# Optimization experiments

Measured on AMD Instinct MI355X. Metric: run time of the kernel, lower is better.

## Reference

```python
import jax, jax.numpy as jnp
import numpy as np

SEQ_LEN = 12          # seq_length
K = 8                 # nsamples = 2 * num_samples
RADII = (4.0 + 1e-06, 8.0 + 1e-06, 12.0 + 1e-06)
COUT = (64, 128, 256)


def _group(xyz, s_xyz, radius):
    # ball query via knn + radius mask: xyz (B,N,3) queries, s_xyz (B,M,3) keys
    d2 = jnp.sum((xyz[:, :, None, :] - s_xyz[:, None, :, :]) ** 2, axis=-1)  # (B,N,M)
    neg, idx = jax.lax.top_k(-d2, K)                                          # (B,N,K)
    valid = (-neg) <= radius * radius
    # points outside the ball are replaced by the nearest neighbor (pad-with-first)
    return jnp.where(valid, idx, idx[..., :1])


def _gather(a, idx):
    # a (B,M,C), idx (B,N,K) -> (B,N,K,C)
    return jax.vmap(lambda t, i: t[i])(a, idx)


def _cell(xyz, feat, state, W, b, radius, cout):
    # PointRNN cell: group state points around current points, fuse
    # [displacement, current feature, state feature] with a shared linear,
    # then max-pool over the K neighbors. New state xyz = current xyz.
    B, N, _ = xyz.shape
    if state is None:
        s_xyz, s_feat = xyz, jnp.zeros((B, N, cout), xyz.dtype)
    else:
        s_xyz, s_feat = state
    idx = _group(xyz, s_xyz, radius)
    n_xyz = _gather(s_xyz, idx)                      # (B,N,K,3)
    n_feat = _gather(s_feat, idx)                    # (B,N,K,cout)
    disp = n_xyz - xyz[:, :, None, :]
    parts = [disp]
    if feat is not None:
        cin = feat.shape[-1]
        parts.append(jnp.broadcast_to(feat[:, :, None, :], (B, N, K, cin)))
    parts.append(n_feat)
    h = jnp.concatenate(parts, axis=-1) @ W + b      # (B,N,K,cout)
    return (xyz, jnp.max(h, axis=2))                 # (xyz, (B,N,cout))


def _forward(frames, W1, b1, W2, b2, W3, b3, Wm, bm, Wl, bl):
    half = SEQ_LEN // 2
    s1 = s2 = s3 = None
    # encode
    for i in range(half):
        s1 = _cell(frames[:, i], None, s1, W1, b1, RADII[0], COUT[0])
        s2 = _cell(s1[0], s1[1], s2, W2, b2, RADII[1], COUT[1])
        s3 = _cell(s2[0], s2[1], s3, W3, b3, RADII[2], COUT[2])
    # decode
    input_frame = frames[:, half - 1]
    preds = []
    for i in range(half, SEQ_LEN):
        s1 = _cell(input_frame, None, s1, W1, b1, RADII[0], COUT[0])
        s2 = _cell(s1[0], s1[1], s2, W2, b2, RADII[1], COUT[1])
        s3 = _cell(s2[0], s2[1], s3, W3, b3, RADII[2], COUT[2])
        h = jax.nn.relu(s3[1] @ Wm + bm)             # MLP([256,64]) = Lin+ReLU
        motion = h @ Wl + bl                         # (B,N,3)
        input_frame = input_frame + motion
        preds.append(input_frame)
    return jnp.stack(preds, axis=1)                  # (B, T/2, N, 3)


def setup_inputs() -> dict:
    key = jax.random.key(0)
    ks = jax.random.split(key, 12)
    B, N = 16, 512
    frames = jax.random.normal(ks[0], (B, SEQ_LEN, N, 3), jnp.float32) * 2.0

    def lin(k, fin, fout):
        k1, k2 = jax.random.split(k)
        s = 1.0 / np.sqrt(fin)
        return (jax.random.uniform(k1, (fin, fout), jnp.float32, -s, s),
                jax.random.uniform(k2, (fout,), jnp.float32, -s, s))

    W1, b1 = lin(ks[1], 3 + 0 + 64, 64)
    W2, b2 = lin(ks[2], 3 + 64 + 128, 128)
    W3, b3 = lin(ks[3], 3 + 128 + 256, 256)
    Wm, bm = lin(ks[4], 256, 64)
    Wl, bl = lin(ks[5], 64, 3)
    return {"frames": frames, "W1": W1, "b1": b1, "W2": W2, "b2": b2,
            "W3": W3, "b3": b3, "Wm": Wm, "bm": bm, "Wl": Wl, "bl": bl}


def reference(frames, W1, b1, W2, b2, W3, b3, Wm, bm, Wl, bl):
    return _forward(frames, W1, b1, W2, b2, W3, b3, Wm, bm, Wl, bl)
```

## Files before the change

kernel.cpp:

```cpp
#include <hip/hip_runtime.h>
#include <hip/hip_cooperative_groups.h>
#include <math.h>

namespace cg = cooperative_groups;

#define BB 16
#define NN 512
#define KNN 8
#define SEQ 12
#define TQK 16
#define QB 32
#define PB 16

typedef __attribute__((ext_vector_type(8))) short bf8_t;
typedef __attribute__((ext_vector_type(4))) float f4_t;

__device__ __forceinline__ ushort f2b(float x) {
    uint u = __float_as_uint(x);
    return (ushort)((u + 0x7fffu + ((u >> 16) & 1u)) >> 16);
}
__device__ __forceinline__ float b2f(ushort h) {
    return __uint_as_float((uint)h << 16);
}

struct CellsSM {
    float s2s[PB][132];
    float s3f[PB][260];
    float dsp[3][PB][KNN][3];
    int   jss[3][PB][KNN];
    union { ushort s1b[2][PB][72]; float hs[PB][64]; } u1;
    ushort s2b[2][PB][136];
    ushort s3c[2][PB][264];
};
union __align__(16) SM {
    CellsSM c;
    ushort  g[384 * 40];
    float   kf[1544 + 4608 + 4608];
};
union __align__(16) GKSM {
    ushort  g[384 * 40];
    float   kf[1544 + 4608 + 4608];
};

#define GRPN 64
__device__ __forceinline__ void group_barrier(int* __restrict__ bar, int g,
                                              int target, int tid) {
    __syncthreads();
    if (tid == 0) {
        __threadfence();
        atomicAdd(&bar[g * 32], 1);
        while (__hip_atomic_load(&bar[g * 32], __ATOMIC_ACQUIRE,
                                 __HIP_MEMORY_SCOPE_AGENT) < target)
            __builtin_amdgcn_s_sleep(2);
        __threadfence();
    }
    __syncthreads();
}

__device__ __forceinline__ void knn512(
        const float* __restrict__ xqp, int xq_bs,
        const float* __restrict__ xsp, int xs_bs,
        int* __restrict__ idx1, int* __restrict__ idx2, int* __restrict__ idx3,
        float r2a, float r2b, float r2c,
        int ntile, int b, float* __restrict__ smf) {
    float* s   = smf;
    float* cdp = smf + 1544;
    int*   cip = (int*)(smf + 1544 + 4608);
    const int tid = threadIdx.x;

    {
        int j = tid;
        const float* p = xsp + (long)b * xs_bs + j * 3;
        int o = 3 * j + (j >> 6);
        s[o + 0] = p[0]; s[o + 1] = p[1]; s[o + 2] = p[2];
    }
    __syncthreads();

    int qi  = tid >> 4;
    int sub = tid & 15;
    int n = ntile * QB + qi;
    const float* q = xqp + (long)b * xq_bs + n * 3;
    float qx = q[0], qy = q[1], qz2 = q[2];

    float bd[KNN];
    int   bi[KNN];
#pragma unroll
    for (int k = 0; k < KNN; ++k) { bd[k] = 1e30f; bi[k] = 0; }

    int j0 = sub * (NN / TQK);
    int sbase = 3 * j0 + (j0 >> 6);
#pragma unroll 4
    for (int jj = 0; jj < NN / TQK; ++jj) {
        float dx = s[sbase + 3 * jj + 0] - qx;
        float dy = s[sbase + 3 * jj + 1] - qy;
        float dz = s[sbase + 3 * jj + 2] - qz2;
        float d2 = fmaf(dx, dx, fmaf(dy, dy, dz * dz));
        if (d2 < bd[KNN - 1]) {
            bd[KNN - 1] = d2; bi[KNN - 1] = j0 + jj;
#pragma unroll
            for (int k = KNN - 1; k >= 1; --k) {
                if (bd[k] < bd[k - 1]) {
                    float td = bd[k]; bd[k] = bd[k - 1]; bd[k - 1] = td;
                    int   ti = bi[k]; bi[k] = bi[k - 1]; bi[k - 1] = ti;
                }
            }
        }
    }

    float* cdq = cdp + (qi * TQK + sub) * (KNN + 1);
    int*   ciq = cip + (qi * TQK + sub) * (KNN + 1);
#pragma unroll
    for (int k = 0; k < KNN; ++k) { cdq[k] = bd[k]; ciq[k] = bi[k]; }
    cdq[KNN] = 1e30f; ciq[KNN] = 0x7fffffff;
    __syncthreads();

    for (int stride = TQK / 2; stride >= 1; stride >>= 1) {
        if (sub < stride) {
            float* ca = cdp + (qi * TQK + sub) * (KNN + 1);
            float* cb = cdp + (qi * TQK + sub + stride) * (KNN + 1);
            int*   ja_p = cip + (qi * TQK + sub) * (KNN + 1);
            int*   jb_p = cip + (qi * TQK + sub + stride) * (KNN + 1);
            float rd[KNN]; int ri[KNN];
            int ia = 0, ib = 0;
#pragma unroll
            for (int k = 0; k < KNN; ++k) {
                float da = ca[ia], db = cb[ib];
                int   ja = ja_p[ia], jb = jb_p[ib];
                bool ta = (da < db) || (da == db && ja < jb);
                rd[k] = ta ? da : db; ri[k] = ta ? ja : jb;
                ia += ta ? 1 : 0; ib += ta ? 0 : 1;
            }
#pragma unroll
            for (int k = 0; k < KNN; ++k) { ca[k] = rd[k]; ja_p[k] = ri[k]; }
        }
        __syncthreads();
    }

    if (sub == 0) {
        long base = ((long)(b * NN + n)) * KNN;
        float* c0  = cdp + qi * TQK * (KNN + 1);
        int*   j0p = cip + qi * TQK * (KNN + 1);
        int i0 = j0p[0];
#pragma unroll
        for (int k = 0; k < KNN; ++k) {
            float d = c0[k]; int j = j0p[k];
            idx1[base + k] = (d <= r2a) ? j : i0;
            idx2[base + k] = (d <= r2b) ? j : i0;
            idx3[base + k] = (d <= r2c) ? j : i0;
        }
    }
}

template<int N>
__device__ __forceinline__ void gemmTile512(
        const ushort* __restrict__ Ah, const ushort* __restrict__ Al,
        const ushort* __restrict__ Bh, const ushort* __restrict__ Bl,
        float* __restrict__ G, int rb, int cb, int tid, ushort* lds) {
    const int row0 = rb * 128, c0 = cb * 64;
    ushort* ah = lds;
    ushort* al = lds + 128 * 40;
    ushort* bh = lds + 256 * 40;
    ushort* bl = lds + 320 * 40;
    const int wv = tid >> 6, lane = tid & 63;
    const int m = lane & 15, quad = lane >> 4;
    const int lr = tid >> 2, ls = (tid & 3) * 8;
    const int lrB = lr & 63;
    ushort* bstage = (tid < 256) ? bh : bl;
    const ushort* Bsrc = (tid < 256) ? Bh : Bl;

    f4_t acc[4];
#pragma unroll
    for (int ct = 0; ct < 4; ++ct) acc[ct] = (f4_t){0.f, 0.f, 0.f, 0.f};

    bf8_t pa_h = *(const bf8_t*)(Ah + (long)(row0 + lr) * N + ls);
    bf8_t pa_l = *(const bf8_t*)(Al + (long)(row0 + lr) * N + ls);
    bf8_t pb   = *(const bf8_t*)(Bsrc + (long)(c0 + lrB) * N + ls);

    for (int k0 = 0; k0 < N; k0 += 32) {
        __syncthreads();
        *(bf8_t*)(ah + lr * 40 + ls) = pa_h;
        *(bf8_t*)(al + lr * 40 + ls) = pa_l;
        *(bf8_t*)(bstage + lrB * 40 + ls) = pb;
        __syncthreads();
        if (k0 + 32 < N) {
            int kn = k0 + 32;
            pa_h = *(const bf8_t*)(Ah + (long)(row0 + lr) * N + kn + ls);
            pa_l = *(const bf8_t*)(Al + (long)(row0 + lr) * N + kn + ls);
            pb   = *(const bf8_t*)(Bsrc + (long)(c0 + lrB) * N + kn + ls);
        }
        bf8_t a_h = *(const bf8_t*)(ah + (wv * 16 + m) * 40 + quad * 8);
        bf8_t a_l = *(const bf8_t*)(al + (wv * 16 + m) * 40 + quad * 8);
#pragma unroll
        for (int ct = 0; ct < 4; ++ct) {
            bf8_t bth = *(const bf8_t*)(bh + (ct * 16 + m) * 40 + quad * 8);
            bf8_t btl = *(const bf8_t*)(bl + (ct * 16 + m) * 40 + quad * 8);
            acc[ct] = __builtin_amdgcn_mfma_f32_16x16x32_bf16(a_h, bth, acc[ct], 0, 0, 0);
            acc[ct] = __builtin_amdgcn_mfma_f32_16x16x32_bf16(a_h, btl, acc[ct], 0, 0, 0);
            acc[ct] = __builtin_amdgcn_mfma_f32_16x16x32_bf16(a_l, bth, acc[ct], 0, 0, 0);
        }
    }
#pragma unroll
    for (int ct = 0; ct < 4; ++ct) {
        int col = c0 + ct * 16 + m;
#pragma unroll
        for (int r = 0; r < 4; ++r)
            G[(long)(row0 + wv * 16 + quad * 4 + r) * N + col] = acc[ct][r];
    }
}

__device__ __forceinline__ void cells_phase(
        bool first,
        const float* __restrict__ xq, int xq_bs,
        const float* __restrict__ xs, int xs_bs,
        const int* __restrict__ i1, const int* __restrict__ i2,
        const int* __restrict__ i3,
        const float* __restrict__ G1p, const float* __restrict__ G2p,
        const float* __restrict__ G3p,
        ushort* __restrict__ s1h, ushort* __restrict__ s1l,
        ushort* __restrict__ s2h, ushort* __restrict__ s2l,
        ushort* __restrict__ s3h, ushort* __restrict__ s3l,
        const float* __restrict__ W1, const float* __restrict__ b1,
        const float* __restrict__ W2, const float* __restrict__ b2,
        const float* __restrict__ W3, const float* __restrict__ b3,
        const ushort* __restrict__ w2fh, const ushort* __restrict__ w2fl,
        const ushort* __restrict__ w3fh, const ushort* __restrict__ w3fl,
        const ushort* __restrict__ wmh, const ushort* __restrict__ wml,
        const float* __restrict__ bm,
        const float* __restrict__ Wl, const float* __restrict__ bl,
        float* __restrict__ xnext, int xn_bs, int do_head,
        int blk, int tid, CellsSM& sm) {
    const int xcd = blk & 7, slot = blk >> 3;
    const int b   = xcd * 2 + (slot >> 5);
    const int n0  = (slot & 31) << 4;
    const long row0 = (long)b * NN + n0;
    const long bN = (long)b * NN;
    const int wv = tid >> 6, lane = tid & 63;
    const int fm = lane & 15, quad = lane >> 4;

    for (int t = tid; t < 3 * PB * KNN; t += 512) {
        int r = t >> 7, rem = t & 127, p = rem >> 3, k = rem & 7;
        const int* ix = (r == 0) ? i1 : ((r == 1) ? i2 : i3);
        int j = ix[(row0 + p) * KNN + k];
        sm.jss[r][p][k] = j;
        const float* sp = xs + (long)b * xs_bs + j * 3;
        const float* qp = xq + (long)b * xq_bs + (n0 + p) * 3;
        sm.dsp[r][p][k][0] = sp[0] - qp[0];
        sm.dsp[r][p][k][1] = sp[1] - qp[1];
        sm.dsp[r][p][k][2] = sp[2] - qp[2];
    }
    __syncthreads();

    {
        int co = tid & 63, q = tid >> 6;
        float g1r[2][KNN];
        if (!first) {
#pragma unroll
            for (int r = 0; r < 2; ++r)
#pragma unroll
                for (int k = 0; k < KNN; ++k)
                    g1r[r][k] = G1p[(bN + sm.jss[0][2 * q + r][k]) * 64 + co];
        }
        float wx = W1[co], wy = W1[64 + co], wz = W1[128 + co];
        float bz = b1[co];
#pragma unroll
        for (int r = 0; r < 2; ++r) {
            int p = 2 * q + r;
            float acc = -1e30f;
#pragma unroll
            for (int k = 0; k < KNN; ++k) {
                float v = fmaf(sm.dsp[0][p][k][0], wx, bz);
                v = fmaf(sm.dsp[0][p][k][1], wy, v);
                v = fmaf(sm.dsp[0][p][k][2], wz, v);
                if (!first) v += g1r[r][k];
                acc = fmaxf(acc, v);
            }
            ushort h = f2b(acc);
            ushort l = f2b(acc - b2f(h));
            sm.u1.s1b[0][p][co] = h;
            sm.u1.s1b[1][p][co] = l;
            s1h[(row0 + p) * 64 + co] = h;
            s1l[(row0 + p) * 64 + co] = l;
        }
    }
    __syncthreads();

    float4 g2r[KNN];
    {
        int c4 = tid & 31, g = tid >> 5;
        if (!first) {
#pragma unroll
            for (int k = 0; k < KNN; ++k)
                g2r[k] = ((const float4*)G2p)[(bN + sm.jss[1][g][k]) * 32 + c4];
        }
    }

    {
        int col = wv * 16 + fm;
        float bz = b2[col];
        f4_t acc = {bz, bz, bz, bz};
#pragma unroll
        for (int k0 = 0; k0 < 64; k0 += 32) {
            bf8_t ah = *(const bf8_t*)&sm.u1.s1b[0][fm][k0 + quad * 8];
            bf8_t al = *(const bf8_t*)&sm.u1.s1b[1][fm][k0 + quad * 8];
            bf8_t bh = *(const bf8_t*)(w2fh + col * 64 + k0 + quad * 8);
            bf8_t bl = *(const bf8_t*)(w2fl + col * 64 + k0 + quad * 8);
            acc = __builtin_amdgcn_mfma_f32_16x16x32_bf16(ah, bh, acc, 0, 0, 0);
            acc = __builtin_amdgcn_mfma_f32_16x16x32_bf16(ah, bl, acc, 0, 0, 0);
            acc = __builtin_amdgcn_mfma_f32_16x16x32_bf16(al, bh, acc, 0, 0, 0);
        }
#pragma unroll
        for (int r = 0; r < 4; ++r) sm.s2s[quad * 4 + r][col] = acc[r];
    }
    __syncthreads();

    {
        int c4 = tid & 31, g = tid >> 5;
        float4 bse = *(float4*)&sm.s2s[g][c4 * 4];
        float4 wx = ((const float4*)W2)[c4];
        float4 wy = ((const float4*)(W2 + 128))[c4];
        float4 wz = ((const float4*)(W2 + 256))[c4];
        float4 m = make_float4(-1e30f, -1e30f, -1e30f, -1e30f);
#pragma unroll
        for (int k = 0; k < KNN; ++k) {
            float dx = sm.dsp[1][g][k][0], dy = sm.dsp[1][g][k][1],
                  dz = sm.dsp[1][g][k][2];
            float4 v;
            v.x = fmaf(dz, wz.x, fmaf(dy, wy.x, fmaf(dx, wx.x, bse.x)));
            v.y = fmaf(dz, wz.y, fmaf(dy, wy.y, fmaf(dx, wx.y, bse.y)));
            v.z = fmaf(dz, wz.z, fmaf(dy, wy.z, fmaf(dx, wx.z, bse.z)));
            v.w = fmaf(dz, wz.w, fmaf(dy, wy.w, fmaf(dx, wx.w, bse.w)));
            if (!first) {
                v.x += g2r[k].x; v.y += g2r[k].y;
                v.z += g2r[k].z; v.w += g2r[k].w;
            }
            m.x = fmaxf(m.x, v.x); m.y = fmaxf(m.y, v.y);
            m.z = fmaxf(m.z, v.z); m.w = fmaxf(m.w, v.w);
        }
        ushort4 mh, ml;
        mh.x = f2b(m.x); ml.x = f2b(m.x - b2f(mh.x));
        mh.y = f2b(m.y); ml.y = f2b(m.y - b2f(mh.y));
        mh.z = f2b(m.z); ml.z = f2b(m.z - b2f(mh.z));
        mh.w = f2b(m.w); ml.w = f2b(m.w - b2f(mh.w));
        *(ushort4*)&sm.s2b[0][g][c4 * 4] = mh;
        *(ushort4*)&sm.s2b[1][g][c4 * 4] = ml;
        *(ushort4*)&s2h[(row0 + g) * 128 + c4 * 4] = mh;
        *(ushort4*)&s2l[(row0 + g) * 128 + c4 * 4] = ml;
    }
    __syncthreads();

    float4 g3r[2][KNN];
    {
        int c4 = tid & 63, g = tid >> 6;
        if (!first) {
#pragma unroll
            for (int r = 0; r < 2; ++r)
#pragma unroll
                for (int k = 0; k < KNN; ++k)
                    g3r[r][k] = ((const float4*)G3p)[(bN + sm.jss[2][2 * g + r][k]) * 64 + c4];
        }
    }

    {
        int col0 = wv * 16 + fm, col1 = (wv + 8) * 16 + fm;
        float bz0 = b3[col0], bz1 = b3[col1];
        f4_t a0 = {bz0, bz0, bz0, bz0};
        f4_t a1 = {bz1, bz1, bz1, bz1};
#pragma unroll
        for (int k0 = 0; k0 < 128; k0 += 32) {
            bf8_t ah = *(const bf8_t*)&sm.s2b[0][fm][k0 + quad * 8];
            bf8_t al = *(const bf8_t*)&sm.s2b[1][fm][k0 + quad * 8];
            bf8_t b0h = *(const bf8_t*)(w3fh + col0 * 128 + k0 + quad * 8);
            bf8_t b0l = *(const bf8_t*)(w3fl + col0 * 128 + k0 + quad * 8);
            bf8_t b1h = *(const bf8_t*)(w3fh + col1 * 128 + k0 + quad * 8);
            bf8_t b1l = *(const bf8_t*)(w3fl + col1 * 128 + k0 + quad * 8);
            a0 = __builtin_amdgcn_mfma_f32_16x16x32_bf16(ah, b0h, a0, 0, 0, 0);
            a0 = __builtin_amdgcn_mfma_f32_16x16x32_bf16(ah, b0l, a0, 0, 0, 0);
            a0 = __builtin_amdgcn_mfma_f32_16x16x32_bf16(al, b0h, a0, 0, 0, 0);
            a1 = __builtin_amdgcn_mfma_f32_16x16x32_bf16(ah, b1h, a1, 0, 0, 0);
            a1 = __builtin_amdgcn_mfma_f32_16x16x32_bf16(ah, b1l, a1, 0, 0, 0);
            a1 = __builtin_amdgcn_mfma_f32_16x16x32_bf16(al, b1h, a1, 0, 0, 0);
        }
#pragma unroll
        for (int r = 0; r < 4; ++r) {
            sm.s3f[quad * 4 + r][col0] = a0[r];
            sm.s3f[quad * 4 + r][col1] = a1[r];
        }
    }
    __syncthreads();

    {
        int c4 = tid & 63, g = tid >> 6;
        float4 wx = ((const float4*)W3)[c4];
        float4 wy = ((const float4*)(W3 + 256))[c4];
        float4 wz = ((const float4*)(W3 + 512))[c4];
#pragma unroll
        for (int r = 0; r < 2; ++r) {
            int p = 2 * g + r;
            float4 bse = *(float4*)&sm.s3f[p][c4 * 4];
            float4 m = make_float4(-1e30f, -1e30f, -1e30f, -1e30f);
#pragma unroll
            for (int k = 0; k < KNN; ++k) {
                float dx = sm.dsp[2][p][k][0], dy = sm.dsp[2][p][k][1],
                      dz = sm.dsp[2][p][k][2];
                float4 v;
                v.x = fmaf(dz, wz.x, fmaf(dy, wy.x, fmaf(dx, wx.x, bse.x)));
                v.y = fmaf(dz, wz.y, fmaf(dy, wy.y, fmaf(dx, wx.y, bse.y)));
                v.z = fmaf(dz, wz.z, fmaf(dy, wy.z, fmaf(dx, wx.z, bse.z)));
                v.w = fmaf(dz, wz.w, fmaf(dy, wy.w, fmaf(dx, wx.w, bse.w)));
                if (!first) {
                    v.x += g3r[r][k].x; v.y += g3r[r][k].y;
                    v.z += g3r[r][k].z; v.w += g3r[r][k].w;
                }
                m.x = fmaxf(m.x, v.x); m.y = fmaxf(m.y, v.y);
                m.z = fmaxf(m.z, v.z); m.w = fmaxf(m.w, v.w);
            }
            ushort4 mh, ml;
            mh.x = f2b(m.x); ml.x = f2b(m.x - b2f(mh.x));
            mh.y = f2b(m.y); ml.y = f2b(m.y - b2f(mh.y));
            mh.z = f2b(m.z); ml.z = f2b(m.z - b2f(mh.z));
            mh.w = f2b(m.w); ml.w = f2b(m.w - b2f(mh.w));
            *(ushort4*)&sm.s3c[0][p][c4 * 4] = mh;
            *(ushort4*)&sm.s3c[1][p][c4 * 4] = ml;
            *(ushort4*)&s3h[(row0 + p) * 256 + c4 * 4] = mh;
            *(ushort4*)&s3l[(row0 + p) * 256 + c4 * 4] = ml;
        }
    }

    if (do_head) {
        __syncthreads();
        if (wv < 4) {
            int col = wv * 16 + fm;
            float bz = bm[col];
            f4_t acc = {bz, bz, bz, bz};
#pragma unroll
            for (int k0 = 0; k0 < 256; k0 += 32) {
                bf8_t ah = *(const bf8_t*)&sm.s3c[0][fm][k0 + quad * 8];
                bf8_t al = *(const bf8_t*)&sm.s3c[1][fm][k0 + quad * 8];
                bf8_t bh = *(const bf8_t*)(wmh + col * 256 + k0 + quad * 8);
                bf8_t bl = *(const bf8_t*)(wml + col * 256 + k0 + quad * 8);
                acc = __builtin_amdgcn_mfma_f32_16x16x32_bf16(ah, bh, acc, 0, 0, 0);
                acc = __builtin_amdgcn_mfma_f32_16x16x32_bf16(ah, bl, acc, 0, 0, 0);
                acc = __builtin_amdgcn_mfma_f32_16x16x32_bf16(al, bh, acc, 0, 0, 0);
            }
            __syncthreads();
#pragma unroll
            for (int r = 0; r < 4; ++r)
                sm.u1.hs[quad * 4 + r][col] = fmaxf(acc[r], 0.f);
        } else {
            __syncthreads();
        }
        __syncthreads();
        if (tid < PB * 3) {
            int p = tid / 3, d = tid % 3;
            float m = bl[d];
#pragma unroll 4
            for (int c = 0; c < 64; ++c)
                m = fmaf(sm.u1.hs[p][c], Wl[c * 3 + d], m);
            const float* qp = xq + (long)b * xq_bs + (n0 + p) * 3;
            xnext[(long)b * xn_bs + (n0 + p) * 3 + d] = qp[d] + m;
        }
    }
}

__device__ __forceinline__ void convW_one(int id,
        const float* __restrict__ W1, const float* __restrict__ W2,
        const float* __restrict__ W3, const float* __restrict__ Wm,
        ushort* w1h, ushort* w1l, ushort* w2h, ushort* w2l,
        ushort* w3h, ushort* w3l, ushort* w2fh, ushort* w2fl,
        ushort* w3fh, ushort* w3fl, ushort* wmh, ushort* wml) {
    float v; ushort* ph; ushort* pl; int idx;
    if (id < 4096)        { int n = id >> 6, k = id & 63;
        v = W1[(3 + k) * 64 + n];   ph = w1h;  pl = w1l;  idx = id; }
    else if (id < 20480)  { int u = id - 4096, n = u >> 7, k = u & 127;
        v = W2[(67 + k) * 128 + n]; ph = w2h;  pl = w2l;  idx = u; }
    else if (id < 86016)  { int u = id - 20480, n = u >> 8, k = u & 255;
        v = W3[(131 + k) * 256 + n]; ph = w3h; pl = w3l;  idx = u; }
    else if (id < 94208)  { int u = id - 86016, n = u >> 6, k = u & 63;
        v = W2[(3 + k) * 128 + n];  ph = w2fh; pl = w2fl; idx = u; }
    else if (id < 126976) { int u = id - 94208, n = u >> 7, k = u & 127;
        v = W3[(3 + k) * 256 + n];  ph = w3fh; pl = w3fl; idx = u; }
    else if (id < 143360) { int u = id - 126976, n = u >> 8, k = u & 255;
        v = Wm[k * 64 + n];         ph = wmh;  pl = wml;  idx = u; }
    else return;
    ushort h = f2b(v);
    ph[idx] = h; pl[idx] = f2b(v - b2f(h));
}

__global__ __launch_bounds__(512, 4) void fused_kernel(
        const float* frames, float* out,
        float* G1, float* G2, float* G3,
        ushort* s1h, ushort* s1l, ushort* s2h, ushort* s2l,
        ushort* s3h, ushort* s3l,
        ushort* w1h, ushort* w1l, ushort* w2h, ushort* w2l,
        ushort* w3h, ushort* w3l,
        ushort* w2fh, ushort* w2fl, ushort* w3fh, ushort* w3fl,
        ushort* wmh, ushort* wml,
        int* idx1w, int* idx2w, int* idx3w, int* bar,
        const float* W1, const float* b1, const float* W2, const float* b2,
        const float* W3, const float* b3, const float* Wm, const float* bm,
        const float* Wl, const float* bl,
        float r2a, float r2b, float r2c) {
    __shared__ SM sm;
    cg::grid_group grid = cg::this_grid();
    const int bx = blockIdx.x, tid = threadIdx.x;
    const int grp = bx & 7;
    const int FB = SEQ * NN * 3, OB = 6 * NN * 3;
    const long BNK = (long)BB * NN * KNN;

    if (bx == 0 && tid < 8) bar[tid * 32] = 0;
    convW_one(bx * 512 + tid, W1, W2, W3, Wm,
              w1h, w1l, w2h, w2l, w3h, w3l,
              w2fh, w2fl, w3fh, w3fl, wmh, wml);
    if (bx < 256) {
        int xcd = bx & 7, slot = bx >> 3;
        int b = xcd * 2 + (slot & 1), ntile = slot >> 1;
        knn512(frames, FB, frames, FB, idx1w, idx2w, idx3w,
               r2a, r2b, r2c, ntile, b, sm.kf);
    }
    __threadfence();
    grid.sync();

    int ph = 1;

    for (int t = 0; t < SEQ; ++t) {
        const float* xq; int xq_bs; const float* xs; int xs_bs;
        if (t < 6)       { xq = frames + (long)t * NN * 3;        xq_bs = FB; }
        else if (t == 6) { xq = frames + 5L * NN * 3;             xq_bs = FB; }
        else             { xq = out + (long)(t - 7) * NN * 3;     xq_bs = OB; }
        if (t == 0)      { xs = xq;                               xs_bs = xq_bs; }
        else if (t <= 6) { xs = frames + (long)(t - 1) * NN * 3;  xs_bs = FB; }
        else if (t == 7) { xs = frames + 5L * NN * 3;             xs_bs = FB; }
        else             { xs = out + (long)(t - 8) * NN * 3;     xs_bs = OB; }
        int slot = (t <= 6) ? t : 0;
        const int* i1 = idx1w + slot * BNK;
        const int* i2 = idx2w + slot * BNK;
        const int* i3 = idx3w + slot * BNK;
        int do_head = (t >= 6);
        float* xnext = do_head ? out + (long)(t - 6) * NN * 3 : nullptr;

        cells_phase(t == 0, xq, xq_bs, xs, xs_bs, i1, i2, i3,
                    G1, G2, G3, s1h, s1l, s2h, s2l, s3h, s3l,
                    W1, b1, W2, b2, W3, b3,
                    w2fh, w2fl, w3fh, w3fl, wmh, wml, bm,
                    Wl, bl, xnext, OB, do_head, bx, tid, sm.c);

        if (t == SEQ - 1) break;
        group_barrier(bar, grp, GRPN * ph, tid); ++ph;

        if (bx < 256) {
            int tn = t + 1;
            const float* kq; int kq_bs; const float* ksp; int ks_bs; int kslot;
            if (tn <= 6) {
                int qz = tn < 5 ? tn : 5;
                kq = frames + (long)qz * NN * 3;        kq_bs = FB;
                ksp = frames + (long)(tn - 1) * NN * 3; ks_bs = FB;
                kslot = tn;
            } else {
                kq = out + (long)(tn - 7) * NN * 3;     kq_bs = OB;
                if (tn == 7) { ksp = frames + 5L * NN * 3;          ks_bs = FB; }
                else         { ksp = out + (long)(tn - 8) * NN * 3; ks_bs = OB; }
                kslot = 0;
            }
            int xcd = bx & 7, slot2 = bx >> 3;
            int b = xcd * 2 + (slot2 & 1), ntile = slot2 >> 1;
            knn512(kq, kq_bs, ksp, ks_bs,
                   idx1w + (long)kslot * BNK, idx2w + (long)kslot * BNK,
                   idx3w + (long)kslot * BNK,
                   r2a, r2b, r2c, ntile, b, sm.kf);
        } else {
            for (int it = bx - 256; it < 448; it += 256) {
                if (it < 256) {
                    int xcd = it & 7, rem = it >> 3;
                    int rb = xcd * 8 + (rem & 7), cb = rem >> 3;
                    gemmTile512<256>(s3h, s3l, w3h, w3l, G3, rb, cb, tid, sm.g);
                } else if (it < 384) {
                    int u = it - 256; int xcd = u & 7, rem = u >> 3;
                    int rb = xcd * 8 + (rem & 7), cb = rem >> 3;
                    gemmTile512<128>(s2h, s2l, w2h, w2l, G2, rb, cb, tid, sm.g);
                } else {
                    int u = it - 384; int xcd = u & 7, j = u >> 3;
                    gemmTile512<64>(s1h, s1l, w1h, w1l, G1, xcd * 8 + j, 0, tid, sm.g);
                }
            }
        }
        group_barrier(bar, grp, GRPN * ph, tid); ++ph;
    }
}

__global__ __launch_bounds__(512) void init512_kernel(
        const float* __restrict__ frames, int FB,
        int* __restrict__ i1, int* __restrict__ i2, int* __restrict__ i3,
        float r2a, float r2b, float r2c,
        const float* __restrict__ W1, const float* __restrict__ W2,
        const float* __restrict__ W3, const float* __restrict__ Wm,
        ushort* w1h, ushort* w1l, ushort* w2h, ushort* w2l,
        ushort* w3h, ushort* w3l, ushort* w2fh, ushort* w2fl,
        ushort* w3fh, ushort* w3fl, ushort* wmh, ushort* wml) {
    __shared__ float kf[1544 + 4608 + 4608];
    int bx = blockIdx.x;
    if (bx < 256) {
        int xcd = bx & 7, slot = bx >> 3;
        int b = xcd * 2 + (slot & 1), ntile = slot >> 1;
        knn512(frames, FB, frames, FB, i1, i2, i3, r2a, r2b, r2c,
               ntile, b, kf);
        return;
    }
    convW_one((bx - 256) * 512 + threadIdx.x, W1, W2, W3, Wm,
              w1h, w1l, w2h, w2l, w3h, w3l,
              w2fh, w2fl, w3fh, w3fl, wmh, wml);
}

__global__ __launch_bounds__(512) void cells512_kernel(
        int first,
        const float* __restrict__ xq, int xq_bs,
        const float* __restrict__ xs, int xs_bs,
        const int* __restrict__ i1, const int* __restrict__ i2,
        const int* __restrict__ i3,
        const float* __restrict__ G1p, const float* __restrict__ G2p,
        const float* __restrict__ G3p,
        ushort* s1h, ushort* s1l, ushort* s2h, ushort* s2l,
        ushort* s3h, ushort* s3l,
        const float* __restrict__ W1, const float* __restrict__ b1,
        const float* __restrict__ W2, const float* __restrict__ b2,
        const float* __restrict__ W3, const float* __restrict__ b3,
        const ushort* __restrict__ w2fh, const ushort* __restrict__ w2fl,
        const ushort* __restrict__ w3fh, const ushort* __restrict__ w3fl,
        const ushort* __restrict__ wmh, const ushort* __restrict__ wml,
        const float* __restrict__ bm,
        const float* __restrict__ Wl, const float* __restrict__ bl,
        float* xnext, int xn_bs, int do_head) {
    __shared__ CellsSM sm;
    cells_phase(first != 0, xq, xq_bs, xs, xs_bs, i1, i2, i3,
                G1p, G2p, G3p, s1h, s1l, s2h, s2l, s3h, s3l,
                W1, b1, W2, b2, W3, b3, w2fh, w2fl, w3fh, w3fl,
                wmh, wml, bm, Wl, bl, xnext, xn_bs, do_head,
                blockIdx.x, threadIdx.x, sm);
}

__global__ __launch_bounds__(512) void gemmknn512_kernel(
        const ushort* s1h, const ushort* s1l,
        const ushort* s2h, const ushort* s2l,
        const ushort* s3h, const ushort* s3l,
        const ushort* w1h, const ushort* w1l,
        const ushort* w2h, const ushort* w2l,
        const ushort* w3h, const ushort* w3l,
        float* G1, float* G2, float* G3,
        const float* __restrict__ kq, int kq_bs,
        const float* __restrict__ ks, int ks_bs,
        int* ki1, int* ki2, int* ki3,
        float r2a, float r2b, float r2c) {
    __shared__ GKSM sm;
    int bx = blockIdx.x, tid = threadIdx.x;
    if (bx < 256) {
        int xcd = bx & 7, slot = bx >> 3;
        int b = xcd * 2 + (slot & 1), ntile = slot >> 1;
        knn512(kq, kq_bs, ks, ks_bs, ki1, ki2, ki3, r2a, r2b, r2c,
               ntile, b, sm.kf);
        return;
    }
    int it = bx - 256;
    if (it < 256) {
        int xcd = it & 7, rem = it >> 3;
        int rb = xcd * 8 + (rem & 7), cb = rem >> 3;
        gemmTile512<256>(s3h, s3l, w3h, w3l, G3, rb, cb, tid, sm.g);
    } else if (it < 384) {
        int u = it - 256; int xcd = u & 7, rem = u >> 3;
        int rb = xcd * 8 + (rem & 7), cb = rem >> 3;
        gemmTile512<128>(s2h, s2l, w2h, w2l, G2, rb, cb, tid, sm.g);
    } else {
        int u = it - 384; int xcd = u & 7, j = u >> 3;
        gemmTile512<64>(s1h, s1l, w1h, w1l, G1, xcd * 8 + j, 0, tid, sm.g);
    }
}

extern "C" void kernel_launch(void* const* d_in, const int* in_sizes, int n_in,
                              void* d_out, int out_size, void* d_ws, size_t ws_size,
                              hipStream_t stream) {
    const float* frames = (const float*)d_in[0];
    const float* W1 = (const float*)d_in[1]; const float* b1 = (const float*)d_in[2];
    const float* W2 = (const float*)d_in[3]; const float* b2 = (const float*)d_in[4];
    const float* W3 = (const float*)d_in[5]; const float* b3 = (const float*)d_in[6];
    const float* Wm = (const float*)d_in[7]; const float* bm = (const float*)d_in[8];
    const float* Wl = (const float*)d_in[9]; const float* bl = (const float*)d_in[10];
    float* out = (float*)d_out;

    const long M = (long)BB * NN;
    float* ws = (float*)d_ws;
    float* G1b = ws; ws += M * 64;
    float* G2b = ws; ws += M * 128;
    float* G3b = ws; ws += M * 256;
    ushort* us = (ushort*)ws;
    ushort* s1h = us; us += M * 64;   ushort* s1l = us; us += M * 64;
    ushort* s2h = us; us += M * 128;  ushort* s2l = us; us += M * 128;
    ushort* s3h = us; us += M * 256;  ushort* s3l = us; us += M * 256;
    ushort* w1h = us; us += 4096;     ushort* w1l = us; us += 4096;
    ushort* w2h = us; us += 16384;    ushort* w2l = us; us += 16384;
    ushort* w3h = us; us += 65536;    ushort* w3l = us; us += 65536;
    ushort* w2fh = us; us += 8192;    ushort* w2fl = us; us += 8192;
    ushort* w3fh = us; us += 32768;   ushort* w3fl = us; us += 32768;
    ushort* wmh = us; us += 16384;    ushort* wml = us; us += 16384;
    const long BNK = M * KNN;
    int* ip = (int*)us;
    int* idx1w = ip; ip += 7 * BNK;
    int* idx2w = ip; ip += 7 * BNK;
    int* idx3w = ip; ip += 7 * BNK;
    int* bar   = ip; ip += 8 * 32;

    double ra = 4.0 + 1e-6, rbd = 8.0 + 1e-6, rc = 12.0 + 1e-6;
    float r2a = (float)(ra * ra), r2b = (float)(rbd * rbd), r2c = (float)(rc * rc);

    const int FB = SEQ * NN * 3;
    const int OB = 6 * NN * 3;

    static int g_coop = -1;
    if (g_coop < 0) {
        int attr = 0, dev = 0, nb = 0;
        hipGetDevice(&dev);
        hipDeviceGetAttribute(&attr, hipDeviceAttributeCooperativeLaunch, dev);
        hipDeviceProp_t prop{};
        hipGetDeviceProperties(&prop, dev);
        if (attr &&
            hipOccupancyMaxActiveBlocksPerMultiprocessor(
                &nb, fused_kernel, 512, 0) == hipSuccess &&
            nb * prop.multiProcessorCount >= 512)
            g_coop = 1;
        else
            g_coop = 0;
    }

    bool did_coop = false;
    if (g_coop == 1) {
        void* args[] = {
            (void*)&frames, (void*)&out,
            (void*)&G1b, (void*)&G2b, (void*)&G3b,
            (void*)&s1h, (void*)&s1l, (void*)&s2h, (void*)&s2l,
            (void*)&s3h, (void*)&s3l,
            (void*)&w1h, (void*)&w1l, (void*)&w2h, (void*)&w2l,
            (void*)&w3h, (void*)&w3l,
            (void*)&w2fh, (void*)&w2fl, (void*)&w3fh, (void*)&w3fl,
            (void*)&wmh, (void*)&wml,
            (void*)&idx1w, (void*)&idx2w, (void*)&idx3w, (void*)&bar,
            (void*)&W1, (void*)&b1, (void*)&W2, (void*)&b2,
            (void*)&W3, (void*)&b3, (void*)&Wm, (void*)&bm,
            (void*)&Wl, (void*)&bl,
            (void*)&r2a, (void*)&r2b, (void*)&r2c
        };
        hipError_t e = hipLaunchCooperativeKernel((const void*)fused_kernel,
                                                  dim3(512), dim3(512),
                                                  args, 0, stream);
        did_coop = (e == hipSuccess);
        if (!did_coop) g_coop = 0;
    }

    if (!did_coop) {
        init512_kernel<<<536, 512, 0, stream>>>(
            frames, FB, idx1w, idx2w, idx3w, r2a, r2b, r2c,
            W1, W2, W3, Wm, w1h, w1l, w2h, w2l, w3h, w3l,
            w2fh, w2fl, w3fh, w3fl, wmh, wml);

        for (int t = 0; t < SEQ; ++t) {
            const float* xq; int xq_bs; const float* xs; int xs_bs;
            if (t < 6)       { xq = frames + (long)t * NN * 3;        xq_bs = FB; }
            else if (t == 6) { xq = frames + 5L * NN * 3;             xq_bs = FB; }
            else             { xq = out + (long)(t - 7) * NN * 3;     xq_bs = OB; }
            if (t == 0)      { xs = xq;                               xs_bs = xq_bs; }
            else if (t <= 6) { xs = frames + (long)(t - 1) * NN * 3;  xs_bs = FB; }
            else if (t == 7) { xs = frames + 5L * NN * 3;             xs_bs = FB; }
            else             { xs = out + (long)(t - 8) * NN * 3;     xs_bs = OB; }

            int slot = (t <= 6) ? t : 0;
            int* i1 = idx1w + (long)slot * BNK;
            int* i2 = idx2w + (long)slot * BNK;
            int* i3 = idx3w + (long)slot * BNK;

            int do_head = (t >= 6);
            float* xnext = do_head ? out + (long)(t - 6) * NN * 3 : nullptr;

            cells512_kernel<<<BB * NN / PB, 512, 0, stream>>>(
                t == 0 ? 1 : 0, xq, xq_bs, xs, xs_bs, i1, i2, i3,
                G1b, G2b, G3b, s1h, s1l, s2h, s2l, s3h, s3l,
                W1, b1, W2, b2, W3, b3,
                w2fh, w2fl, w3fh, w3fl, wmh, wml, bm,
                Wl, bl, xnext, OB, do_head);

            if (t < SEQ - 1) {
                int tn = t + 1;
                const float* kq; int kq_bs; const float* ksp; int ks_bs; int kslot;
                if (tn <= 6) {
                    int qz = tn < 5 ? tn : 5;
                    kq = frames + (long)qz * NN * 3;        kq_bs = FB;
                    ksp = frames + (long)(tn - 1) * NN * 3; ks_bs = FB;
                    kslot = tn;
                } else {
                    kq = out + (long)(tn - 7) * NN * 3;     kq_bs = OB;
                    if (tn == 7) { ksp = frames + 5L * NN * 3;          ks_bs = FB; }
                    else         { ksp = out + (long)(tn - 8) * NN * 3; ks_bs = OB; }
                    kslot = 0;
                }
                gemmknn512_kernel<<<704, 512, 0, stream>>>(
                    s1h, s1l, s2h, s2l, s3h, s3l,
                    w1h, w1l, w2h, w2l, w3h, w3l,
                    G1b, G2b, G3b,
                    kq, kq_bs, ksp, ks_bs,
                    idx1w + (long)kslot * BNK, idx2w + (long)kslot * BNK,
                    idx3w + (long)kslot * BNK,
                    r2a, r2b, r2c);
            }
        }
    }
}
```

Baseline: 531.8 us.

## Widen GEMM tiles to 128 columns and add nontemporal loads/stores

The split-bf16 GEMM tile is generalized to 128 output columns for the layer-2 and layer-3 state GEMMs, so each A-tile load feeds twice as many MFMAs. The GEMM tile count drops from 448 to 256, and the fused gemm+knn launch shrinks from 704 to 512 blocks. Index and state writes and reads now use nontemporal builtins to avoid polluting caches. The trade-off is fewer, heavier blocks with more accumulator registers and more LDS, which may lower occupancy and the parallelism available for the GEMM phase.

```diff
diff --git a/kernel.cpp b/kernel.cpp
--- a/kernel.cpp
+++ b/kernel.cpp
@@ -14,6 +14,7 @@
 
 typedef __attribute__((ext_vector_type(8))) short bf8_t;
 typedef __attribute__((ext_vector_type(4))) float f4_t;
+typedef __attribute__((ext_vector_type(4))) ushort u4_t;
 
 __device__ __forceinline__ ushort f2b(float x) {
     uint u = __float_as_uint(x);
@@ -21,6 +22,24 @@
 }
 __device__ __forceinline__ float b2f(ushort h) {
     return __uint_as_float((uint)h << 16);
+}
+
+__device__ __forceinline__ void nts_us(ushort* p, ushort v) {
+    __builtin_nontemporal_store(v, p);
+}
+__device__ __forceinline__ void nts_u4(ushort* p, ushort a, ushort b,
+                                       ushort c, ushort d) {
+    u4_t v = {a, b, c, d};
+    __builtin_nontemporal_store(v, (u4_t*)p);
+}
+__device__ __forceinline__ void nts_i(int* p, int v) {
+    __builtin_nontemporal_store(v, p);
+}
+__device__ __forceinline__ int ntl_i(const int* p) {
+    return __builtin_nontemporal_load(p);
+}
+__device__ __forceinline__ bf8_t ntl_b8(const ushort* p) {
+    return __builtin_nontemporal_load((const bf8_t*)p);
 }
 
 struct CellsSM {
@@ -34,11 +53,11 @@
 };
 union __align__(16) SM {
     CellsSM c;
-    ushort  g[384 * 40];
+    ushort  g[256 * 40 + 2 * 128 * 40];
     float   kf[1544 + 4608 + 4608];
 };
 union __align__(16) GKSM {
-    ushort  g[384 * 40];
+    ushort  g[256 * 40 + 2 * 128 * 40];
     float   kf[1544 + 4608 + 4608];
 };
 
@@ -144,54 +163,71 @@
 #pragma unroll
         for (int k = 0; k < KNN; ++k) {
             float d = c0[k]; int j = j0p[k];
-            idx1[base + k] = (d <= r2a) ? j : i0;
-            idx2[base + k] = (d <= r2b) ? j : i0;
-            idx3[base + k] = (d <= r2c) ? j : i0;
-        }
-    }
-}
-
-template<int N>
-__device__ __forceinline__ void gemmTile512(
+            nts_i(&idx1[base + k], (d <= r2a) ? j : i0);
+            nts_i(&idx2[base + k], (d <= r2b) ? j : i0);
+            nts_i(&idx3[base + k], (d <= r2c) ? j : i0);
+        }
+    }
+}
+
+template<int N, int NC>
+__device__ __forceinline__ void gemmTileW(
         const ushort* __restrict__ Ah, const ushort* __restrict__ Al,
         const ushort* __restrict__ Bh, const ushort* __restrict__ Bl,
         float* __restrict__ G, int rb, int cb, int tid, ushort* lds) {
-    const int row0 = rb * 128, c0 = cb * 64;
+    const int row0 = rb * 128, c0 = cb * NC;
     ushort* ah = lds;
     ushort* al = lds + 128 * 40;
     ushort* bh = lds + 256 * 40;
-    ushort* bl = lds + 320 * 40;
+    ushort* bl = lds + 256 * 40 + NC * 40;
     const int wv = tid >> 6, lane = tid & 63;
     const int m = lane & 15, quad = lane >> 4;
     const int lr = tid >> 2, ls = (tid & 3) * 8;
-    const int lrB = lr & 63;
-    ushort* bstage = (tid < 256) ? bh : bl;
-    const ushort* Bsrc = (tid < 256) ? Bh : Bl;
-
-    f4_t acc[4];
-#pragma unroll
-    for (int ct = 0; ct < 4; ++ct) acc[ct] = (f4_t){0.f, 0.f, 0.f, 0.f};
-
-    bf8_t pa_h = *(const bf8_t*)(Ah + (long)(row0 + lr) * N + ls);
-    bf8_t pa_l = *(const bf8_t*)(Al + (long)(row0 + lr) * N + ls);
-    bf8_t pb   = *(const bf8_t*)(Bsrc + (long)(c0 + lrB) * N + ls);
+
+    f4_t acc[NC / 16];
+#pragma unroll
+    for (int ct = 0; ct < NC / 16; ++ct) acc[ct] = (f4_t){0.f, 0.f, 0.f, 0.f};
+
+    bf8_t pa_h = ntl_b8(Ah + (long)(row0 + lr) * N + ls);
+    bf8_t pa_l = ntl_b8(Al + (long)(row0 + lr) * N + ls);
+    bf8_t pb_h, pb_l;
+    const int lrB = (NC == 128) ? lr : (lr & 63);
+    if (NC == 128) {
+        pb_h = *(const bf8_t*)(Bh + (long)(c0 + lrB) * N + ls);
+        pb_l = *(const bf8_t*)(Bl + (long)(c0 + lrB) * N + ls);
+    } else {
+        const ushort* Bs = (tid < 256) ? Bh : Bl;
+        pb_h = *(const bf8_t*)(Bs + (long)(c0 + lrB) * N + ls);
+    }
 
     for (int k0 = 0; k0 < N; k0 += 32) {
         __syncthreads();
         *(bf8_t*)(ah + lr * 40 + ls) = pa_h;
         *(bf8_t*)(al + lr * 40 + ls) = pa_l;
-        *(bf8_t*)(bstage + lrB * 40 + ls) = pb;
+        if (NC == 128) {
+            *(bf8_t*)(bh + lrB * 40 + ls) = pb_h;
+            *(bf8_t*)(bl + lrB * 40 + ls) = pb_l;
+        } else {
+            ushort* bs = (tid < 256) ? bh : bl;
+            *(bf8_t*)(bs + lrB * 40 + ls) = pb_h;
+        }
         __syncthreads();
         if (k0 + 32 < N) {
             int kn = k0 + 32;
-            pa_h = *(const bf8_t*)(Ah + (long)(row0 + lr) * N + kn + ls);
-            pa_l = *(const bf8_t*)(Al + (long)(row0 + lr) * N + kn + ls);
-            pb   = *(const bf8_t*)(Bsrc + (long)(c0 + lrB) * N + kn + ls);
+            pa_h = ntl_b8(Ah + (long)(row0 + lr) * N + kn + ls);
+            pa_l = ntl_b8(Al + (long)(row0 + lr) * N + kn + ls);
+            if (NC == 128) {
+                pb_h = *(const bf8_t*)(Bh + (long)(c0 + lrB) * N + kn + ls);
+                pb_l = *(const bf8_t*)(Bl + (long)(c0 + lrB) * N + kn + ls);
+            } else {
+                const ushort* Bs = (tid < 256) ? Bh : Bl;
+                pb_h = *(const bf8_t*)(Bs + (long)(c0 + lrB) * N + kn + ls);
+            }
         }
         bf8_t a_h = *(const bf8_t*)(ah + (wv * 16 + m) * 40 + quad * 8);
         bf8_t a_l = *(const bf8_t*)(al + (wv * 16 + m) * 40 + quad * 8);
 #pragma unroll
-        for (int ct = 0; ct < 4; ++ct) {
+        for (int ct = 0; ct < NC / 16; ++ct) {
             bf8_t bth = *(const bf8_t*)(bh + (ct * 16 + m) * 40 + quad * 8);
             bf8_t btl = *(const bf8_t*)(bl + (ct * 16 + m) * 40 + quad * 8);
             acc[ct] = __builtin_amdgcn_mfma_f32_16x16x32_bf16(a_h, bth, acc[ct], 0, 0, 0);
@@ -200,12 +236,33 @@
         }
     }
 #pragma unroll
-    for (int ct = 0; ct < 4; ++ct) {
+    for (int ct = 0; ct < NC / 16; ++ct) {
         int col = c0 + ct * 16 + m;
 #pragma unroll
         for (int r = 0; r < 4; ++r)
             G[(long)(row0 + wv * 16 + quad * 4 + r) * N + col] = acc[ct][r];
     }
+}
+
+__device__ __forceinline__ void gemm_dispatch(
+        int it, int tid, ushort* lds,
+        const ushort* s1h, const ushort* s1l,
+        const ushort* s2h, const ushort* s2l,
+        const ushort* s3h, const ushort* s3l,
+        const ushort* w1h, const ushort* w1l,
+        const ushort* w2h, const ushort* w2l,
+        const ushort* w3h, const ushort* w3l,
+        float* G1, float* G2, float* G3) {
+    int g = it & 7, j = it >> 3;
+    if (j < 16)
+        gemmTileW<256, 128>(s3h, s3l, w3h, w3l, G3, g * 8 + (j & 7), j >> 3,
+                            tid, lds);
+    else if (j < 24)
+        gemmTileW<128, 128>(s2h, s2l, w2h, w2l, G2, g * 8 + (j - 16), 0,
+                            tid, lds);
+    else
+        gemmTileW<64, 64>(s1h, s1l, w1h, w1l, G1, g * 8 + (j - 24), 0,
+                          tid, lds);
 }
 
 __device__ __forceinline__ void cells_phase(
@@ -240,7 +297,7 @@
     for (int t = tid; t < 3 * PB * KNN; t += 512) {
         int r = t >> 7, rem = t & 127, p = rem >> 3, k = rem & 7;
         const int* ix = (r == 0) ? i1 : ((r == 1) ? i2 : i3);
-        int j = ix[(row0 + p) * KNN + k];
+        int j = ntl_i(&ix[(row0 + p) * KNN + k]);
         sm.jss[r][p][k] = j;
         const float* sp = xs + (long)b * xs_bs + j * 3;
         const float* qp = xq + (long)b * xq_bs + (n0 + p) * 3;
@@ -278,8 +335,8 @@
             ushort l = f2b(acc - b2f(h));
             sm.u1.s1b[0][p][co] = h;
             sm.u1.s1b[1][p][co] = l;
-            s1h[(row0 + p) * 64 + co] = h;
-            s1l[(row0 + p) * 64 + co] = l;
+            nts_us(&s1h[(row0 + p) * 64 + co], h);
+            nts_us(&s1l[(row0 + p) * 64 + co], l);
         }
     }
     __syncthreads();
@@ -343,8 +400,8 @@
         mh.w = f2b(m.w); ml.w = f2b(m.w - b2f(mh.w));
         *(ushort4*)&sm.s2b[0][g][c4 * 4] = mh;
         *(ushort4*)&sm.s2b[1][g][c4 * 4] = ml;
-        *(ushort4*)&s2h[(row0 + g) * 128 + c4 * 4] = mh;
-        *(ushort4*)&s2l[(row0 + g) * 128 + c4 * 4] = ml;
+        nts_u4(&s2h[(row0 + g) * 128 + c4 * 4], mh.x, mh.y, mh.z, mh.w);
+        nts_u4(&s2l[(row0 + g) * 128 + c4 * 4], ml.x, ml.y, ml.z, ml.w);
     }
     __syncthreads();
 
@@ -421,8 +478,8 @@
             mh.w = f2b(m.w); ml.w = f2b(m.w - b2f(mh.w));
             *(ushort4*)&sm.s3c[0][p][c4 * 4] = mh;
             *(ushort4*)&sm.s3c[1][p][c4 * 4] = ml;
-            *(ushort4*)&s3h[(row0 + p) * 256 + c4 * 4] = mh;
-            *(ushort4*)&s3l[(row0 + p) * 256 + c4 * 4] = ml;
+            nts_u4(&s3h[(row0 + p) * 256 + c4 * 4], mh.x, mh.y, mh.z, mh.w);
+            nts_u4(&s3l[(row0 + p) * 256 + c4 * 4], ml.x, ml.y, ml.z, ml.w);
         }
     }
 
@@ -568,20 +625,9 @@
                    idx3w + (long)kslot * BNK,
                    r2a, r2b, r2c, ntile, b, sm.kf);
         } else {
-            for (int it = bx - 256; it < 448; it += 256) {
-                if (it < 256) {
-                    int xcd = it & 7, rem = it >> 3;
-                    int rb = xcd * 8 + (rem & 7), cb = rem >> 3;
-                    gemmTile512<256>(s3h, s3l, w3h, w3l, G3, rb, cb, tid, sm.g);
-                } else if (it < 384) {
-                    int u = it - 256; int xcd = u & 7, rem = u >> 3;
-                    int rb = xcd * 8 + (rem & 7), cb = rem >> 3;
-                    gemmTile512<128>(s2h, s2l, w2h, w2l, G2, rb, cb, tid, sm.g);
-                } else {
-                    int u = it - 384; int xcd = u & 7, j = u >> 3;
-                    gemmTile512<64>(s1h, s1l, w1h, w1l, G1, xcd * 8 + j, 0, tid, sm.g);
-                }
-            }
+            gemm_dispatch(bx - 256, tid, sm.g,
+                          s1h, s1l, s2h, s2l, s3h, s3l,
+                          w1h, w1l, w2h, w2l, w3h, w3l, G1, G2, G3);
         }
         group_barrier(bar, grp, GRPN * ph, tid); ++ph;
     }
@@ -658,19 +704,9 @@
                ntile, b, sm.kf);
         return;
     }
-    int it = bx - 256;
-    if (it < 256) {
-        int xcd = it & 7, rem = it >> 3;
-        int rb = xcd * 8 + (rem & 7), cb = rem >> 3;
-        gemmTile512<256>(s3h, s3l, w3h, w3l, G3, rb, cb, tid, sm.g);
-    } else if (it < 384) {
-        int u = it - 256; int xcd = u & 7, rem = u >> 3;
-        int rb = xcd * 8 + (rem & 7), cb = rem >> 3;
-        gemmTile512<128>(s2h, s2l, w2h, w2l, G2, rb, cb, tid, sm.g);
-    } else {
-        int u = it - 384; int xcd = u & 7, j = u >> 3;
-        gemmTile512<64>(s1h, s1l, w1h, w1l, G1, xcd * 8 + j, 0, tid, sm.g);
-    }
+    gemm_dispatch(bx - 256, tid, sm.g,
+                  s1h, s1l, s2h, s2l, s3h, s3l,
+                  w1h, w1l, w2h, w2l, w3h, w3l, G1, G2, G3);
 }
 
 extern "C" void kernel_launch(void* const* d_in, const int* in_sizes, int n_in,
@@ -797,7 +833,7 @@
                     else         { ksp = out + (long)(tn - 8) * NN * 3; ks_bs = OB; }
                     kslot = 0;
                 }
-                gemmknn512_kernel<<<704, 512, 0, stream>>>(
+                gemmknn512_kernel<<<512, 512, 0, stream>>>(
                     s1h, s1l, s2h, s2l, s3h, s3l,
                     w1h, w1l, w2h, w2l, w3h, w3l,
                     G1b, G2b, G3b,
```

Result: no change. 538.2 us (+1.2%).
